# Kernel optimization log

Hardware: AMD Instinct MI355X
Metric: run time of the kernel (lower is better)

Reference implementation:

```python
import jax, jax.numpy as jnp
import numpy as np

B, S, D, H = 4, 2048, 1024, 16
DH = D // H


def setup_inputs() -> dict:
    key = jax.random.key(0)
    k0, k1, k2, k3 = jax.random.split(key, 4)
    x = jax.random.normal(k0, (B, S, D), dtype=jnp.float32)
    k = jax.random.normal(k1, (B, H, S, DH), dtype=jnp.float32)
    v = jax.random.normal(k2, (B, H, S, DH), dtype=jnp.float32)
    # nn.Linear(d, d, bias=False) weight: [out, in]; scaled like torch default init
    Wq = jax.random.normal(k3, (D, D), dtype=jnp.float32) * (1.0 / np.sqrt(D))
    return {"x": x, "k": k, "v": v, "Wq": Wq}


def reference(x, k, v, Wq):
    Bx, Sx, d = x.shape
    h, dh = k.shape[1], k.shape[3]
    rd = jnp.sqrt(jnp.float32(d))  # NOTE: module scales by sqrt(d), not sqrt(d_head)
    # q projection: y = x @ Wq.T  -> [B,S,d] -> [B,h,S,dh]
    q = (x @ Wq.T).reshape(Bx, Sx, h, dh).transpose(0, 2, 1, 3)
    # scores [B,h,S,S]
    a = jnp.einsum('bhqd,bhkd->bhqk', q, k) / rd
    causal = jnp.triu(jnp.ones((Sx, Sx), dtype=bool), k=1)
    a = jnp.where(causal, -jnp.inf, a)
    p = jax.nn.softmax(a, axis=-1)
    o = jnp.einsum('bhqk,bhkd->bhqd', p, v)  # [B,h,S,dh]
    o = o.transpose(0, 2, 1, 3).reshape(Bx, Sx, d)
    return x + o
```

## Files before the change

### kernel.cpp

```cpp
#include <hip/hip_runtime.h>
#include <hip/hip_bf16.h>

typedef __attribute__((ext_vector_type(4))) float f32x4;
typedef __attribute__((ext_vector_type(8))) short bf16x8;
typedef __attribute__((ext_vector_type(4))) unsigned short u16x4;

#define MFMA16(a, b, c) __builtin_amdgcn_mfma_f32_16x16x32_bf16((a), (b), (c), 0, 0, 0)

static __device__ __forceinline__ unsigned short f2bf(float f) {
    unsigned u = __float_as_uint(f);
    u += 0x7FFFu + ((u >> 16) & 1u);
    return (unsigned short)(u >> 16);
}
static __device__ __forceinline__ uint2 pack4_rhu(float4 v) {
    unsigned a = __float_as_uint(v.x) + 0x8000u;
    unsigned b = __float_as_uint(v.y) + 0x8000u;
    unsigned c = __float_as_uint(v.z) + 0x8000u;
    unsigned d = __float_as_uint(v.w) + 0x8000u;
    uint2 r;
    r.x = __builtin_amdgcn_perm(b, a, 0x07060302u);
    r.y = __builtin_amdgcn_perm(d, c, 0x07060302u);
    return r;
}
static __device__ __forceinline__ float exp2_fast(float x) {
#if __has_builtin(__builtin_amdgcn_exp2f)
    return __builtin_amdgcn_exp2f(x);
#else
    return exp2f(x);
#endif
}

#define QSCALE 0.04508422002778011f

__global__ __launch_bounds__(256) void prep_kernel(const float* __restrict__ x,
                                                   const float* __restrict__ wq,
                                                   const float* __restrict__ kin,
                                                   const float* __restrict__ vin,
                                                   unsigned short* __restrict__ qout,
                                                   unsigned short* __restrict__ kb,
                                                   unsigned short* __restrict__ vt) {
    __shared__ __align__(16) unsigned short As[2][128][40];
    __shared__ __align__(16) unsigned short Bs[2][128][40];
    const int bid = blockIdx.x;
    const int tid = threadIdx.x;

    if (bid < 512) {
        const int m0 = (bid & 63) * 128;
        const int n0 = (bid >> 6) * 128;
        const int wave = tid >> 6, lane = tid & 63;
        const int lg = lane >> 4, lc = lane & 15;
        const int wm = wave >> 1, wn = wave & 1;

        f32x4 acc[4][4];
#pragma unroll
        for (int i = 0; i < 4; ++i)
#pragma unroll
            for (int j = 0; j < 4; ++j) acc[i][j] = (f32x4){0.f, 0.f, 0.f, 0.f};

        float4 ax[4], bx[4];
#pragma unroll
        for (int i = 0; i < 4; ++i) {
            int c = tid + i * 256;
            int row = c >> 3, kc = (c & 7) * 4;
            ax[i] = *(const float4*)(x  + (size_t)(m0 + row) * 1024 + kc);
            bx[i] = *(const float4*)(wq + (size_t)(n0 + row) * 1024 + kc);
        }
#pragma unroll
        for (int i = 0; i < 4; ++i) {
            int c = tid + i * 256;
            int row = c >> 3, kc = (c & 7) * 4;
            *(uint2*)&As[0][row][kc] = pack4_rhu(ax[i]);
            *(uint2*)&Bs[0][row][kc] = pack4_rhu(bx[i]);
        }

        int cur = 0;
        for (int ki = 0; ki < 32; ++ki) {
            __syncthreads();
            const bool havenext = (ki + 1 < 32);
            if (havenext) {
                int ks = (ki + 1) * 32;
#pragma unroll
                for (int i = 0; i < 4; ++i) {
                    int c = tid + i * 256;
                    int row = c >> 3, kc = (c & 7) * 4;
                    ax[i] = *(const float4*)(x  + (size_t)(m0 + row) * 1024 + ks + kc);
                    bx[i] = *(const float4*)(wq + (size_t)(n0 + row) * 1024 + ks + kc);
                }
            }
            bf16x8 af[4], bfr[4];
#pragma unroll
            for (int i = 0; i < 4; ++i) {
                af[i]  = *(const bf16x8*)&As[cur][wm * 64 + i * 16 + lc][lg * 8];
                bfr[i] = *(const bf16x8*)&Bs[cur][wn * 64 + i * 16 + lc][lg * 8];
            }
            __builtin_amdgcn_s_setprio(1);
#pragma unroll
            for (int mi = 0; mi < 4; ++mi)
#pragma unroll
                for (int ni = 0; ni < 4; ++ni)
                    acc[mi][ni] = MFMA16(af[mi], bfr[ni], acc[mi][ni]);
            __builtin_amdgcn_s_setprio(0);
            if (havenext) {
#pragma unroll
                for (int i = 0; i < 4; ++i) {
                    int c = tid + i * 256;
                    int row = c >> 3, kc = (c & 7) * 4;
                    *(uint2*)&As[cur ^ 1][row][kc] = pack4_rhu(ax[i]);
                    *(uint2*)&Bs[cur ^ 1][row][kc] = pack4_rhu(bx[i]);
                }
            }
            cur ^= 1;
        }
#pragma unroll
        for (int mi = 0; mi < 4; ++mi)
#pragma unroll
            for (int ni = 0; ni < 4; ++ni)
#pragma unroll
                for (int r = 0; r < 4; ++r) {
                    int m = m0 + wm * 64 + mi * 16 + lg * 4 + r;
                    int n = n0 + wn * 64 + ni * 16 + lc;
                    int b = m >> 11, s = m & 2047;
                    int h = n >> 6, dh = n & 63;
                    qout[(((size_t)b * 16 + h) * 2048 + s) * 64 + dh] = f2bf(acc[mi][ni][r] * QSCALE);
                }
    } else if (bid < 512 + 2048) {
        const int base = (bid - 512) * 256 + tid;
        float4 v0 = ((const float4*)kin)[base];
        float4 v1 = ((const float4*)kin)[base + 524288];
        float4 v2 = ((const float4*)kin)[base + 1048576];
        float4 v3 = ((const float4*)kin)[base + 1572864];
        *(uint2*)&((u16x4*)kb)[base]           = pack4_rhu(v0);
        *(uint2*)&((u16x4*)kb)[base + 524288]  = pack4_rhu(v1);
        *(uint2*)&((u16x4*)kb)[base + 1048576] = pack4_rhu(v2);
        *(uint2*)&((u16x4*)kb)[base + 1572864] = pack4_rhu(v3);
    } else {
        float (*buf)[65] = (float (*)[65])(&As[0][0][0]);
        const int idx = bid - (512 + 2048);
        const int s0 = (idx & 31) * 64;
        const int bh = idx >> 5;
#pragma unroll
        for (int i = 0; i < 4; ++i) {
            int c = tid + i * 256;
            int s = c >> 4, dc = (c & 15) * 4;
            float4 val = *(const float4*)(vin + ((size_t)bh * 2048 + s0 + s) * 64 + dc);
            buf[s][dc] = val.x; buf[s][dc + 1] = val.y; buf[s][dc + 2] = val.z; buf[s][dc + 3] = val.w;
        }
        __syncthreads();
#pragma unroll
        for (int i = 0; i < 4; ++i) {
            int c = tid + i * 256;
            int dh = c >> 4, sc = (c & 15) * 4;
            u16x4 o = { f2bf(buf[sc][dh]), f2bf(buf[sc + 1][dh]), f2bf(buf[sc + 2][dh]), f2bf(buf[sc + 3][dh]) };
            *(u16x4*)(vt + ((size_t)bh * 64 + dh) * 2048 + s0 + sc) = o;
        }
    }
}

__global__ __launch_bounds__(256, 3) void attn_kernel(const unsigned short* __restrict__ qg,
                                                      const unsigned short* __restrict__ kg,
                                                      const unsigned short* __restrict__ vtg,
                                                      const float* __restrict__ x,
                                                      float* __restrict__ outp) {
    __shared__ __align__(16) unsigned short Ks[2][64][64];
    __shared__ __align__(16) unsigned short VTs[2][64][64];
    __shared__ __align__(16) unsigned short Ps[4][32][72];

    const int bh = blockIdx.x;
    const int qb = 15 - blockIdx.y;
    const int b = bh >> 4, h = bh & 15;
    const int tid = threadIdx.x;
    const int wave = tid >> 6, lane = tid & 63;
    const int lg = lane >> 4, lc = lane & 15;
    const int lc7 = lc & 7;
    const int qw0 = qb * 128 + wave * 32;
    const int nkv = 2 * qb + 2;

    const int r0  = tid >> 3;
    const int c16 = tid & 7;
    const int swz = (c16 ^ (r0 & 7)) * 8;
    const unsigned short* kbase = kg  + ((size_t)bh * 2048 + r0) * 64 + c16 * 8;
    const unsigned short* vbase = vtg + ((size_t)bh * 64 + r0) * 2048 + c16 * 8;

    bf16x8 qf[2][2];
#pragma unroll
    for (int qt = 0; qt < 2; ++qt)
#pragma unroll
        for (int c = 0; c < 2; ++c)
            qf[qt][c] = *(const bf16x8*)(qg + ((size_t)bh * 2048 + qw0 + qt * 16 + lc) * 64 + c * 32 + lg * 8);

    f32x4 oacc[2][4];
#pragma unroll
    for (int qt = 0; qt < 2; ++qt)
#pragma unroll
        for (int dt = 0; dt < 4; ++dt) oacc[qt][dt] = (f32x4){0.f, 0.f, 0.f, 0.f};
    float l_r[2] = {0.f, 0.f};

    {
        *(bf16x8*)&Ks[0][r0][swz]       = *(const bf16x8*)(kbase);
        *(bf16x8*)&Ks[0][r0 + 32][swz]  = *(const bf16x8*)(kbase + 2048);
        *(bf16x8*)&VTs[0][r0][swz]      = *(const bf16x8*)(vbase);
        *(bf16x8*)&VTs[0][r0 + 32][swz] = *(const bf16x8*)(vbase + 65536);
    }

    int cur = 0;
    for (int kv = 0; kv < nkv; ++kv) {
        __syncthreads();

        const bool havenext = (kv + 1 < nkv);
        const int nxt = havenext ? kv + 1 : kv;
        bf16x8 nk0 = *(const bf16x8*)(kbase + (size_t)nxt * 4096);
        bf16x8 nk1 = *(const bf16x8*)(kbase + (size_t)nxt * 4096 + 2048);
        bf16x8 nv0 = *(const bf16x8*)(vbase + nxt * 64);
        bf16x8 nv1 = *(const bf16x8*)(vbase + nxt * 64 + 65536);

        const bool active = (kv * 64 <= qw0 + 31);
        if (active) {
            bf16x8 kf[4][2];
#pragma unroll
            for (int kt = 0; kt < 4; ++kt)
#pragma unroll
                for (int c = 0; c < 2; ++c)
                    kf[kt][c] = *(const bf16x8*)&Ks[cur][kt * 16 + lc][((4 * c + lg) ^ lc7) * 8];

            const int kvb = kv * 64;
#pragma unroll
            for (int qt = 0; qt < 2; ++qt) {
                f32x4 st[4];
                __builtin_amdgcn_s_setprio(1);
#pragma unroll
                for (int kt = 0; kt < 4; ++kt) {
                    f32x4 a = (f32x4){0.f, 0.f, 0.f, 0.f};
                    a = MFMA16(kf[kt][0], qf[qt][0], a);
                    a = MFMA16(kf[kt][1], qf[qt][1], a);
                    st[kt] = a;
                }
                __builtin_amdgcn_s_setprio(0);

                float pp[4][4];
#pragma unroll
                for (int kt = 0; kt < 4; ++kt)
#pragma unroll
                    for (int r = 0; r < 4; ++r) pp[kt][r] = st[kt][r];
                if (kvb + 63 > qw0 + qt * 16) {
                    const int qrow = qw0 + qt * 16 + lc;
#pragma unroll
                    for (int kt = 0; kt < 4; ++kt)
#pragma unroll
                        for (int r = 0; r < 4; ++r) {
                            int kk = kvb + kt * 16 + lg * 4 + r;
                            if (kk > qrow) pp[kt][r] = -1e30f;
                        }
                }
                float rs = 0.f;
#pragma unroll
                for (int kt = 0; kt < 4; ++kt)
#pragma unroll
                    for (int r = 0; r < 4; ++r) {
                        float e = exp2_fast(pp[kt][r]);
                        pp[kt][r] = e;
                        rs += e;
                    }
                l_r[qt] += rs;
#pragma unroll
                for (int kt = 0; kt < 4; ++kt) {
                    uint2 w;
                    w.x = __builtin_amdgcn_perm(__float_as_uint(pp[kt][1]), __float_as_uint(pp[kt][0]), 0x07060302u);
                    w.y = __builtin_amdgcn_perm(__float_as_uint(pp[kt][3]), __float_as_uint(pp[kt][2]), 0x07060302u);
                    *(uint2*)&Ps[wave][qt * 16 + lc][kt * 16 + lg * 4] = w;
                }
            }
            asm volatile("s_waitcnt lgkmcnt(0)" ::: "memory");

            bf16x8 pf[2][2];
#pragma unroll
            for (int qt = 0; qt < 2; ++qt)
#pragma unroll
                for (int c = 0; c < 2; ++c)
                    pf[qt][c] = *(const bf16x8*)&Ps[wave][qt * 16 + lc][c * 32 + lg * 8];
            __builtin_amdgcn_s_setprio(1);
#pragma unroll
            for (int dt = 0; dt < 4; ++dt)
#pragma unroll
                for (int c = 0; c < 2; ++c) {
                    bf16x8 vtf = *(const bf16x8*)&VTs[cur][dt * 16 + lc][((4 * c + lg) ^ lc7) * 8];
#pragma unroll
                    for (int qt = 0; qt < 2; ++qt)
                        oacc[qt][dt] = MFMA16(vtf, pf[qt][c], oacc[qt][dt]);
                }
            __builtin_amdgcn_s_setprio(0);
        }

        if (havenext) {
            *(bf16x8*)&Ks[cur ^ 1][r0][swz]       = nk0;
            *(bf16x8*)&Ks[cur ^ 1][r0 + 32][swz]  = nk1;
            *(bf16x8*)&VTs[cur ^ 1][r0][swz]      = nv0;
            *(bf16x8*)&VTs[cur ^ 1][r0 + 32][swz] = nv1;
        }
        cur ^= 1;
    }

#pragma unroll
    for (int qt = 0; qt < 2; ++qt) {
        float lt = l_r[qt];
        lt += __shfl_xor(lt, 16, 64);
        lt += __shfl_xor(lt, 32, 64);
        float li = 1.0f / lt;
        const int q = qw0 + qt * 16 + lc;
        const size_t obase = ((size_t)b * 2048 + q) * 1024 + (size_t)h * 64 + lg * 4;
#pragma unroll
        for (int dt = 0; dt < 4; ++dt) {
            const size_t oi = obase + dt * 16;
            float4 xv = *(const float4*)(x + oi);
            float4 ov;
            ov.x = xv.x + oacc[qt][dt][0] * li;
            ov.y = xv.y + oacc[qt][dt][1] * li;
            ov.z = xv.z + oacc[qt][dt][2] * li;
            ov.w = xv.w + oacc[qt][dt][3] * li;
            *(float4*)(outp + oi) = ov;
        }
    }
}

extern "C" void kernel_launch(void* const* d_in, const int* in_sizes, int n_in,
                              void* d_out, int out_size, void* d_ws, size_t ws_size,
                              hipStream_t stream) {
    const float* x  = (const float*)d_in[0];
    const float* k  = (const float*)d_in[1];
    const float* v  = (const float*)d_in[2];
    const float* wq = (const float*)d_in[3];
    float* outp = (float*)d_out;

    const size_t NELEM = (size_t)4 * 2048 * 1024;
    unsigned short* qbuf = (unsigned short*)d_ws;
    unsigned short* kbuf = qbuf + NELEM;
    unsigned short* vtbuf = kbuf + NELEM;

    prep_kernel<<<512 + 2048 + 2048, 256, 0, stream>>>(x, wq, k, v, qbuf, kbuf, vtbuf);
    attn_kernel<<<dim3(64, 16), 256, 0, stream>>>(qbuf, kbuf, vtbuf, x, outp);
}
```

Baseline: 96.86 us.

## Shrink attention blocks to 64 queries with two waves and single-buffered KV

```diff
diff --git a/kernel.cpp b/kernel.cpp
--- a/kernel.cpp
+++ b/kernel.cpp
@@ -156,30 +156,32 @@
     }
 }
 
-__global__ __launch_bounds__(256, 3) void attn_kernel(const unsigned short* __restrict__ qg,
-                                                      const unsigned short* __restrict__ kg,
-                                                      const unsigned short* __restrict__ vtg,
-                                                      const float* __restrict__ x,
-                                                      float* __restrict__ outp) {
-    __shared__ __align__(16) unsigned short Ks[2][64][64];
-    __shared__ __align__(16) unsigned short VTs[2][64][64];
-    __shared__ __align__(16) unsigned short Ps[4][32][72];
+__global__ __launch_bounds__(128) void attn_kernel(const unsigned short* __restrict__ qg,
+                                                   const unsigned short* __restrict__ kg,
+                                                   const unsigned short* __restrict__ vtg,
+                                                   const float* __restrict__ x,
+                                                   float* __restrict__ outp) {
+    __shared__ __align__(16) unsigned short Ks[64][64];
+    __shared__ __align__(16) unsigned short VTs[64][64];
+    __shared__ __align__(16) unsigned short Ps[2][32][72];
 
     const int bh = blockIdx.x;
-    const int qb = 15 - blockIdx.y;
+    const int qblk = 31 - blockIdx.y;
     const int b = bh >> 4, h = bh & 15;
     const int tid = threadIdx.x;
     const int wave = tid >> 6, lane = tid & 63;
     const int lg = lane >> 4, lc = lane & 15;
     const int lc7 = lc & 7;
-    const int qw0 = qb * 128 + wave * 32;
-    const int nkv = 2 * qb + 2;
-
-    const int r0  = tid >> 3;
-    const int c16 = tid & 7;
-    const int swz = (c16 ^ (r0 & 7)) * 8;
-    const unsigned short* kbase = kg  + ((size_t)bh * 2048 + r0) * 64 + c16 * 8;
-    const unsigned short* vbase = vtg + ((size_t)bh * 64 + r0) * 2048 + c16 * 8;
+    const int qw0 = qblk * 64 + wave * 32;
+    const int nkv = qblk + 1;
+
+    const int sr = tid >> 1;
+    const int cb = (tid & 1) * 4;
+    int swz[4];
+#pragma unroll
+    for (int j = 0; j < 4; ++j) swz[j] = ((cb + j) ^ (sr & 7)) * 8;
+    const unsigned short* kbase = kg  + ((size_t)bh * 2048 + sr) * 64;
+    const unsigned short* vbase = vtg + ((size_t)bh * 64 + sr) * 2048;
 
     bf16x8 qf[2][2];
 #pragma unroll
@@ -196,107 +198,107 @@
     float l_r[2] = {0.f, 0.f};
 
     {
-        *(bf16x8*)&Ks[0][r0][swz]       = *(const bf16x8*)(kbase);
-        *(bf16x8*)&Ks[0][r0 + 32][swz]  = *(const bf16x8*)(kbase + 2048);
-        *(bf16x8*)&VTs[0][r0][swz]      = *(const bf16x8*)(vbase);
-        *(bf16x8*)&VTs[0][r0 + 32][swz] = *(const bf16x8*)(vbase + 65536);
+#pragma unroll
+        for (int j = 0; j < 4; ++j) {
+            *(bf16x8*)&Ks[sr][swz[j]]  = *(const bf16x8*)(kbase + (cb + j) * 8);
+            *(bf16x8*)&VTs[sr][swz[j]] = *(const bf16x8*)(vbase + (cb + j) * 8);
+        }
     }
 
-    int cur = 0;
     for (int kv = 0; kv < nkv; ++kv) {
         __syncthreads();
 
         const bool havenext = (kv + 1 < nkv);
         const int nxt = havenext ? kv + 1 : kv;
-        bf16x8 nk0 = *(const bf16x8*)(kbase + (size_t)nxt * 4096);
-        bf16x8 nk1 = *(const bf16x8*)(kbase + (size_t)nxt * 4096 + 2048);
-        bf16x8 nv0 = *(const bf16x8*)(vbase + nxt * 64);
-        bf16x8 nv1 = *(const bf16x8*)(vbase + nxt * 64 + 65536);
-
-        const bool active = (kv * 64 <= qw0 + 31);
-        if (active) {
-            bf16x8 kf[4][2];
+        bf16x8 nk[4], nv[4];
+#pragma unroll
+        for (int j = 0; j < 4; ++j) {
+            nk[j] = *(const bf16x8*)(kbase + (size_t)nxt * 4096 + (cb + j) * 8);
+            nv[j] = *(const bf16x8*)(vbase + nxt * 64 + (cb + j) * 8);
+        }
+
+        bf16x8 kf[4][2];
+#pragma unroll
+        for (int kt = 0; kt < 4; ++kt)
+#pragma unroll
+            for (int c = 0; c < 2; ++c)
+                kf[kt][c] = *(const bf16x8*)&Ks[kt * 16 + lc][((4 * c + lg) ^ lc7) * 8];
+
+        const int kvb = kv * 64;
+#pragma unroll
+        for (int qt = 0; qt < 2; ++qt) {
+            f32x4 st[4];
+            __builtin_amdgcn_s_setprio(1);
+#pragma unroll
+            for (int kt = 0; kt < 4; ++kt) {
+                f32x4 a = (f32x4){0.f, 0.f, 0.f, 0.f};
+                a = MFMA16(kf[kt][0], qf[qt][0], a);
+                a = MFMA16(kf[kt][1], qf[qt][1], a);
+                st[kt] = a;
+            }
+            __builtin_amdgcn_s_setprio(0);
+
+            float pp[4][4];
 #pragma unroll
             for (int kt = 0; kt < 4; ++kt)
 #pragma unroll
-                for (int c = 0; c < 2; ++c)
-                    kf[kt][c] = *(const bf16x8*)&Ks[cur][kt * 16 + lc][((4 * c + lg) ^ lc7) * 8];
-
-            const int kvb = kv * 64;
-#pragma unroll
-            for (int qt = 0; qt < 2; ++qt) {
-                f32x4 st[4];
-                __builtin_amdgcn_s_setprio(1);
-#pragma unroll
-                for (int kt = 0; kt < 4; ++kt) {
-                    f32x4 a = (f32x4){0.f, 0.f, 0.f, 0.f};
-                    a = MFMA16(kf[kt][0], qf[qt][0], a);
-                    a = MFMA16(kf[kt][1], qf[qt][1], a);
-                    st[kt] = a;
+                for (int r = 0; r < 4; ++r) pp[kt][r] = st[kt][r];
+            if (kvb + 63 > qw0 + qt * 16) {
+                const int qrow = qw0 + qt * 16 + lc;
+#pragma unroll
+                for (int kt = 0; kt < 4; ++kt)
+#pragma unroll
+                    for (int r = 0; r < 4; ++r) {
+                        int kk = kvb + kt * 16 + lg * 4 + r;
+                        if (kk > qrow) pp[kt][r] = -1e30f;
+                    }
+            }
+            float rs = 0.f;
+#pragma unroll
+            for (int kt = 0; kt < 4; ++kt)
+#pragma unroll
+                for (int r = 0; r < 4; ++r) {
+                    float e = exp2_fast(pp[kt][r]);
+                    pp[kt][r] = e;
+                    rs += e;
                 }
-                __builtin_amdgcn_s_setprio(0);
-
-                float pp[4][4];
-#pragma unroll
-                for (int kt = 0; kt < 4; ++kt)
-#pragma unroll
-                    for (int r = 0; r < 4; ++r) pp[kt][r] = st[kt][r];
-                if (kvb + 63 > qw0 + qt * 16) {
-                    const int qrow = qw0 + qt * 16 + lc;
-#pragma unroll
-                    for (int kt = 0; kt < 4; ++kt)
-#pragma unroll
-                        for (int r = 0; r < 4; ++r) {
-                            int kk = kvb + kt * 16 + lg * 4 + r;
-                            if (kk > qrow) pp[kt][r] = -1e30f;
-                        }
-                }
-                float rs = 0.f;
-#pragma unroll
-                for (int kt = 0; kt < 4; ++kt)
-#pragma unroll
-                    for (int r = 0; r < 4; ++r) {
-                        float e = exp2_fast(pp[kt][r]);
-                        pp[kt][r] = e;
-                        rs += e;
-                    }
-                l_r[qt] += rs;
-#pragma unroll
-                for (int kt = 0; kt < 4; ++kt) {
-                    uint2 w;
-                    w.x = __builtin_amdgcn_perm(__float_as_uint(pp[kt][1]), __float_as_uint(pp[kt][0]), 0x07060302u);
-                    w.y = __builtin_amdgcn_perm(__float_as_uint(pp[kt][3]), __float_as_uint(pp[kt][2]), 0x07060302u);
-                    *(uint2*)&Ps[wave][qt * 16 + lc][kt * 16 + lg * 4] = w;
-                }
-            }
-            asm volatile("s_waitcnt lgkmcnt(0)" ::: "memory");
-
-            bf16x8 pf[2][2];
-#pragma unroll
-            for (int qt = 0; qt < 2; ++qt)
-#pragma unroll
-                for (int c = 0; c < 2; ++c)
-                    pf[qt][c] = *(const bf16x8*)&Ps[wave][qt * 16 + lc][c * 32 + lg * 8];
-            __builtin_amdgcn_s_setprio(1);
-#pragma unroll
-            for (int dt = 0; dt < 4; ++dt)
-#pragma unroll
-                for (int c = 0; c < 2; ++c) {
-                    bf16x8 vtf = *(const bf16x8*)&VTs[cur][dt * 16 + lc][((4 * c + lg) ^ lc7) * 8];
-#pragma unroll
-                    for (int qt = 0; qt < 2; ++qt)
-                        oacc[qt][dt] = MFMA16(vtf, pf[qt][c], oacc[qt][dt]);
-                }
-            __builtin_amdgcn_s_setprio(0);
-        }
-
+            l_r[qt] += rs;
+#pragma unroll
+            for (int kt = 0; kt < 4; ++kt) {
+                uint2 w;
+                w.x = __builtin_amdgcn_perm(__float_as_uint(pp[kt][1]), __float_as_uint(pp[kt][0]), 0x07060302u);
+                w.y = __builtin_amdgcn_perm(__float_as_uint(pp[kt][3]), __float_as_uint(pp[kt][2]), 0x07060302u);
+                *(uint2*)&Ps[wave][qt * 16 + lc][kt * 16 + lg * 4] = w;
+            }
+        }
+        asm volatile("s_waitcnt lgkmcnt(0)" ::: "memory");
+
+        bf16x8 pf[2][2];
+#pragma unroll
+        for (int qt = 0; qt < 2; ++qt)
+#pragma unroll
+            for (int c = 0; c < 2; ++c)
+                pf[qt][c] = *(const bf16x8*)&Ps[wave][qt * 16 + lc][c * 32 + lg * 8];
+        __builtin_amdgcn_s_setprio(1);
+#pragma unroll
+        for (int dt = 0; dt < 4; ++dt)
+#pragma unroll
+            for (int c = 0; c < 2; ++c) {
+                bf16x8 vtf = *(const bf16x8*)&VTs[dt * 16 + lc][((4 * c + lg) ^ lc7) * 8];
+#pragma unroll
+                for (int qt = 0; qt < 2; ++qt)
+                    oacc[qt][dt] = MFMA16(vtf, pf[qt][c], oacc[qt][dt]);
+            }
+        __builtin_amdgcn_s_setprio(0);
+
+        __syncthreads();
         if (havenext) {
-            *(bf16x8*)&Ks[cur ^ 1][r0][swz]       = nk0;
-            *(bf16x8*)&Ks[cur ^ 1][r0 + 32][swz]  = nk1;
-            *(bf16x8*)&VTs[cur ^ 1][r0][swz]      = nv0;
-            *(bf16x8*)&VTs[cur ^ 1][r0 + 32][swz] = nv1;
-        }
-        cur ^= 1;
+#pragma unroll
+            for (int j = 0; j < 4; ++j) {
+                *(bf16x8*)&Ks[sr][swz[j]]  = nk[j];
+                *(bf16x8*)&VTs[sr][swz[j]] = nv[j];
+            }
+        }
     }
 
 #pragma unroll
@@ -336,5 +338,5 @@
     unsigned short* vtbuf = kbuf + NELEM;
 
     prep_kernel<<<512 + 2048 + 2048, 256, 0, stream>>>(x, wq, k, v, qbuf, kbuf, vtbuf);
-    attn_kernel<<<dim3(64, 16), 256, 0, stream>>>(qbuf, kbuf, vtbuf, x, outp);
-}
+    attn_kernel<<<dim3(64, 32), 128, 0, stream>>>(qbuf, kbuf, vtbuf, x, outp);
+}
```

New measurement: 110.3 us. 13.9% more time.
